# Performance work log

Measured on AMD Instinct MI355X. Metric: run time of the kernel, lower is better.

The kernel has to match this reference:

```python
import jax, jax.numpy as jnp
import numpy as np

B, N, D_MODEL = 2, 2048, 1024
H, HEAD_DIM, D1 = 16, 128, 2048
NK, RANK = 16, 32
GAMMA = 0.999


def setup_inputs() -> dict:
    key = jax.random.key(0)
    ks = jax.random.split(key, 12)
    std = 0.02
    return {
        "x": jax.random.normal(ks[0], (B, N, D_MODEL), jnp.float32),
        "Wu": jax.random.normal(ks[1], (D_MODEL, D1), jnp.float32) * std,
        "bu": jax.random.normal(ks[2], (D1,), jnp.float32) * std,
        "Wv": jax.random.normal(ks[3], (D_MODEL, D1), jnp.float32) * std,
        "bv": jax.random.normal(ks[4], (D1,), jnp.float32) * std,
        "Wo": jax.random.normal(ks[5], (D1, D_MODEL), jnp.float32) * std,
        "bo": jax.random.normal(ks[6], (D_MODEL,), jnp.float32) * std,
        # SKI low-rank Toeplitz kernel factors at nk inducing relative positions
        "a_pos": jax.random.normal(ks[7], (H, NK, RANK), jnp.float32) * 0.1,
        "b_pos": jax.random.normal(ks[8], (H, RANK, HEAD_DIM), jnp.float32) * 0.1,
        "a_neg": jax.random.normal(ks[9], (H, NK, RANK), jnp.float32) * 0.1,
        "b_neg": jax.random.normal(ks[10], (H, RANK, HEAD_DIM), jnp.float32) * 0.1,
        "t_zero": jax.random.normal(ks[11], (H, HEAD_DIM), jnp.float32) * 0.1,
    }


def _interp_decay_kernel(a, b, n):
    # low-rank kernel at nk inducing points: [h, nk, d]
    k_ind = jnp.einsum("hkr,hrd->hkd", a, b)
    lags = jnp.arange(1, n)                      # lags 1..n-1
    p = (lags - 1.0) / (n - 2.0) * (NK - 1)      # map lag onto inducing grid
    lo = jnp.floor(p).astype(jnp.int32)
    hi = jnp.minimum(lo + 1, NK - 1)
    w = (p - lo)[None, :, None]
    k = k_ind[:, lo, :] * (1.0 - w) + k_ind[:, hi, :] * w  # [h, n-1, d]
    decay = (GAMMA ** lags)[None, :, None]
    return k * decay


def reference(x, Wu, bu, Wv, bv, Wo, bo, a_pos, b_pos, a_neg, b_neg, t_zero):
    u = jax.nn.silu(x @ Wu + bu)                 # [b, n, d1]
    v = jax.nn.silu(x @ Wv + bv)                 # [b, n, d1]
    n = v.shape[1]
    vh = v.reshape(v.shape[0], n, H, HEAD_DIM)   # [b, n, h, d]

    kp = _interp_decay_kernel(a_pos, b_pos, n)   # [h, n-1, d]
    kn = _interp_decay_kernel(a_neg, b_neg, n)   # [h, n-1, d]
    m = 2 * n
    k_full = jnp.zeros((H, m, HEAD_DIM), vh.dtype)
    k_full = k_full.at[:, 0].set(t_zero)
    k_full = k_full.at[:, 1:n].set(kp)
    k_full = k_full.at[:, m - jnp.arange(1, n)].set(kn)  # non-causal (negative lags)

    # circular FFT convolution along the sequence axis
    vf = jnp.fft.rfft(vh, n=m, axis=1)                    # [b, mf, h, d]
    kf = jnp.transpose(jnp.fft.rfft(k_full, axis=1), (1, 0, 2))[None]  # [1, mf, h, d]
    y = jnp.fft.irfft(vf * kf, n=m, axis=1)[:, :n]        # [b, n, h, d]

    out = u * y.reshape(y.shape[0], n, D1)                # elementwise gate
    return out @ Wo + bo
```

## Files before the change

kernel.cpp:

```cpp
#include <hip/hip_runtime.h>
#include <hip/hip_bf16.h>
#include <stdint.h>
#include <stddef.h>

#define BB 2
#define NSEQ 2048
#define DM 1024
#define H 16
#define HD 128
#define D1 2048
#define NKI 16
#define RANKI 32
#define MROWS (BB * NSEQ)
#define VPROWS 6144
#define NTAP 28
#define NPAIR 13
#define NCHUNK 128
#define CLEN 16
#define GAMMA_F 0.999f
#define G_CL 0.9841201f
#define LN_G (-1.00050033e-3f)

__device__ constexpr int TAPS[NTAP] = {
  1, 2, 138, 139, 274, 275, 411, 412, 547, 548, 684,
  820, 821, 956, 957, 1093, 1094, 1229, 1230, 1366,
  1502, 1503, 1638, 1639, 1775, 1776, 1911, 1912};
__device__ constexpr int LEADL[NPAIR] = {1, 138, 274, 411, 547, 820, 956, 1093, 1229, 1502, 1638, 1775, 1911};
__device__ constexpr int LEADI[NPAIR] = {0, 2, 4, 6, 8, 11, 13, 15, 17, 20, 22, 24, 26};
#define SGL0_L 684
#define SGL0_I 10
#define SGL1_L 1366
#define SGL1_I 19

typedef short short8 __attribute__((ext_vector_type(8)));
typedef float floatx4 __attribute__((ext_vector_type(4)));

__device__ __forceinline__ float bf2f(unsigned short u) {
  union { unsigned int i; float f; } v; v.i = ((unsigned int)u) << 16; return v.f;
}
__device__ __forceinline__ unsigned short f2bf(float f) {
  union { float f; unsigned int i; } v; v.f = f;
  unsigned int r = (v.i + 0x7FFFu + ((v.i >> 16) & 1u)) >> 16;
  return (unsigned short)r;
}
__device__ __forceinline__ float bflo(unsigned int p) {
  union { unsigned int i; float f; } v; v.i = p << 16; return v.f;
}
__device__ __forceinline__ float bfhi(unsigned int p) {
  union { unsigned int i; float f; } v; v.i = p & 0xffff0000u; return v.f;
}
__device__ __forceinline__ void async16(const unsigned short* g, unsigned short* l) {
  __builtin_amdgcn_global_load_lds(
      (const __attribute__((address_space(1))) unsigned int*)g,
      (__attribute__((address_space(3))) unsigned int*)l, 16, 0, 0);
}

#define CVT4 (MROWS * DM / 4)
#define PAD16 (4 * NSEQ * D1 / 8)
__global__ __launch_bounds__(256) void prep_kernel(const float* __restrict__ x,
                                                   unsigned short* __restrict__ x_bf,
                                                   unsigned short* __restrict__ Vp) {
  int i = blockIdx.x * 256 + threadIdx.x;
  if (i < CVT4) {
    float4 f = ((const float4*)x)[i];
    ushort4 o;
    o.x = f2bf(f.x); o.y = f2bf(f.y); o.z = f2bf(f.z); o.w = f2bf(f.w);
    ((ushort4*)x_bf)[i] = o;
  } else {
    int j = i - CVT4;
    if (j < PAD16) {
      int r = j >> 19;
      int off = j & 524287;
      const size_t bases[4] = {0, (size_t)4096 * D1, (size_t)VPROWS * D1,
                               (size_t)VPROWS * D1 + (size_t)4096 * D1};
      uint4 z; z.x = z.y = z.z = z.w = 0u;
      ((uint4*)(Vp + bases[r]))[off] = z;
    }
  }
}

__device__ __forceinline__ float KinterpL(const float* kk, int l, int d) {
  if (l < 1) return 0.0f;
  float p = (float)(l - 1) * (15.0f / 2046.0f);
  int lo = (int)p; if (lo > 15) lo = 15;
  int hi = lo + 1; if (hi > 15) hi = 15;
  float w = p - (float)lo;
  float v = kk[lo * HD + d] * (1.0f - w) + kk[hi * HD + d] * w;
  return v * __powf(GAMMA_F, (float)l);
}

__global__ __launch_bounds__(256) void wprep_kernel(const float* __restrict__ Wu,
                                                    const float* __restrict__ Wv,
                                                    const float* __restrict__ Wo,
                                                    unsigned short* __restrict__ WT2,
                                                    unsigned short* __restrict__ WoT,
                                                    const float* __restrict__ ap,
                                                    const float* __restrict__ bp,
                                                    const float* __restrict__ an,
                                                    const float* __restrict__ bn,
                                                    float* __restrict__ dtp,
                                                    float* __restrict__ dtn) {
  int blk = blockIdx.x;
  int tid = threadIdx.x;
  if (blk < 6144) {
    __shared__ unsigned short t[32][33];
    const float* in; unsigned short* out;
    int rows, cols, bx, by;
    if (blk < 2048) {
      in = Wo; out = WoT; rows = D1; cols = DM;
      bx = (blk & 31) * 32; by = (blk >> 5) * 32;
    } else {
      int local = blk - 2048;
      int z = local >> 11, l2 = local & 2047;
      in = z ? Wv : Wu; out = WT2 + (size_t)z * D1 * DM;
      rows = DM; cols = D1;
      bx = (l2 & 63) * 32; by = (l2 >> 6) * 32;
    }
    int tx = tid & 31, ty = tid >> 5;
#pragma unroll
    for (int j = 0; j < 32; j += 8)
      t[ty + j][tx] = f2bf(in[(size_t)(by + ty + j) * cols + bx + tx]);
    __syncthreads();
#pragma unroll
    for (int j = 0; j < 32; j += 8)
      out[(size_t)(bx + ty + j) * rows + by + tx] = t[tx][ty + j];
  } else {
    __shared__ float kk[NKI * HD];
    int e0 = blk - 6144;
    int h = e0 & 15, dir = e0 >> 4;
    const float* a = (dir ? an : ap) + h * NKI * RANKI;
    const float* b = (dir ? bn : bp) + h * RANKI * HD;
    for (int e = tid; e < NKI * HD; e += 256) {
      int k = e >> 7, d = e & 127;
      float s = 0.0f;
#pragma unroll
      for (int r = 0; r < RANKI; ++r) s += a[k * RANKI + r] * b[r * HD + d];
      kk[e] = s;
    }
    __syncthreads();
    float* dt = (dir ? dtn : dtp) + (size_t)h * NTAP * HD;
    for (int e = tid; e < NTAP * HD; e += 256) {
      int j = e >> 7, d = e & 127;
      int l = TAPS[j];
      float K0 = KinterpL(kk, l, d);
      float K1 = KinterpL(kk, l - 1, d);
      float K2 = KinterpL(kk, l - 2, d);
      dt[e] = K0 - 2.0f * GAMMA_F * K1 + (GAMMA_F * GAMMA_F) * K2;
    }
  }
}

template <int MTILES>
__global__ __launch_bounds__(256) void gemm_uv(const unsigned short* __restrict__ A,
                                               const unsigned short* __restrict__ Bt,
                                               const float* __restrict__ bias,
                                               const float* __restrict__ bias2,
                                               void* __restrict__ C,
                                               void* __restrict__ C2,
                                               int M, int N, int K,
                                               int do_silu, int c_fp32, int uv_mode) {
  __shared__ unsigned short Al[2][MTILES * 1024];
  __shared__ unsigned short Bl[2][4096];
  int m0 = blockIdx.y * (MTILES * 32), n0 = blockIdx.x * 128;
  int tid = threadIdx.x;
  int lane = tid & 63, w = tid >> 6;
  int rw = (w >> 1) * (MTILES * 16), cw = (w & 1) * 64;
  int q = lane >> 4, l16 = lane & 15;
  floatx4 acc[MTILES][4];
#pragma unroll
  for (int mt = 0; mt < MTILES; ++mt)
#pragma unroll
    for (int nt = 0; nt < 4; ++nt) acc[mt][nt] = (floatx4){0.f, 0.f, 0.f, 0.f};
  int grow = tid >> 2;
  int gcol = (tid & 3) * 8;
  const unsigned short* A0 = A + (size_t)(m0 + grow) * K + gcol;
  const unsigned short* A1 = A0 + (size_t)64 * K;
  const unsigned short* B0 = Bt + (size_t)(n0 + grow) * K + gcol;
  const unsigned short* B1 = B0 + (size_t)64 * K;
  int woff = w * 512;
  int nIter = K >> 5;
  async16(A0, &Al[0][woff]);
  if (MTILES == 4) async16(A1, &Al[0][2048 + woff]);
  async16(B0, &Bl[0][woff]);
  async16(B1, &Bl[0][2048 + woff]);
  int p = 0;
  for (int i = 0; i < nIter; ++i) {
    __syncthreads();
    if (i + 1 < nIter) {
      int kn = (i + 1) << 5;
      async16(A0 + kn, &Al[p ^ 1][woff]);
      if (MTILES == 4) async16(A1 + kn, &Al[p ^ 1][2048 + woff]);
      async16(B0 + kn, &Bl[p ^ 1][woff]);
      async16(B1 + kn, &Bl[p ^ 1][2048 + woff]);
    }
    short8 af[MTILES], bfr[4];
#pragma unroll
    for (int i4 = 0; i4 < MTILES; ++i4)
      af[i4] = *(const short8*)(&Al[p][(rw + i4 * 16 + l16) * 32 + q * 8]);
#pragma unroll
    for (int i4 = 0; i4 < 4; ++i4)
      bfr[i4] = *(const short8*)(&Bl[p][(cw + i4 * 16 + l16) * 32 + q * 8]);
#pragma unroll
    for (int mt = 0; mt < MTILES; ++mt)
#pragma unroll
      for (int nt = 0; nt < 4; ++nt)
        acc[mt][nt] = __builtin_amdgcn_mfma_f32_16x16x32_bf16(af[mt], bfr[nt], acc[mt][nt], 0, 0, 0);
    p ^= 1;
  }
  int isv = uv_mode && (n0 >= 2048);
  int ldc = uv_mode ? 2048 : N;
  int ncb = isv ? (n0 - 2048) : n0;
  const float* buse = isv ? bias2 : bias;
#pragma unroll
  for (int mt = 0; mt < MTILES; ++mt) {
#pragma unroll
    for (int nt = 0; nt < 4; ++nt) {
      int n = ncb + cw + nt * 16 + l16;
      float bsv = buse[n];
#pragma unroll
      for (int r = 0; r < 4; ++r) {
        int m = m0 + rw + mt * 16 + q * 4 + r;
        float val = acc[mt][nt][r] + bsv;
        if (do_silu) val = val / (1.0f + __expf(-val));
        if (isv) {
          size_t mrow = (size_t)(2048 + m + ((m >> 11) << 12));
          ((unsigned short*)C2)[mrow * 2048 + n] = f2bf(val);
        } else if (c_fp32) {
          ((float*)C)[(size_t)m * ldc + n] = val;
        } else {
          ((unsigned short*)C)[(size_t)m * ldc + n] = f2bf(val);
        }
      }
    }
  }
}

template <int MTILES, int KCH>
__global__ __launch_bounds__(256) void gemm_out(const unsigned short* __restrict__ A,
                                                const unsigned short* __restrict__ Bt,
                                                const float* __restrict__ bias,
                                                float* __restrict__ C,
                                                int M, int N, int K) {
  constexpr int AREG = MTILES * 1024;
  constexpr int BREG = 4096;
  __shared__ unsigned short Al[2][AREG * KCH];
  __shared__ unsigned short Bl[2][BREG * KCH];
  int m0 = blockIdx.y * (MTILES * 32), n0 = blockIdx.x * 128;
  int tid = threadIdx.x;
  int lane = tid & 63, w = tid >> 6;
  int rw = (w >> 1) * (MTILES * 16), cw = (w & 1) * 64;
  int q = lane >> 4, l16 = lane & 15;
  floatx4 acc[MTILES][4];
#pragma unroll
  for (int mt = 0; mt < MTILES; ++mt)
#pragma unroll
    for (int nt = 0; nt < 4; ++nt) acc[mt][nt] = (floatx4){0.f, 0.f, 0.f, 0.f};
  int grow = tid >> 2;
  int gcol = (tid & 3) * 8;
  const unsigned short* A0 = A + (size_t)(m0 + grow) * K + gcol;
  const unsigned short* A1 = A0 + (size_t)64 * K;
  const unsigned short* B0 = Bt + (size_t)(n0 + grow) * K + gcol;
  const unsigned short* B1 = B0 + (size_t)64 * K;
  int woff = w * 512;
  int nIter = K / (32 * KCH);
#pragma unroll
  for (int kc = 0; kc < KCH; ++kc) {
    async16(A0 + kc * 32, &Al[0][kc * AREG + woff]);
    if (MTILES == 4) async16(A1 + kc * 32, &Al[0][kc * AREG + 2048 + woff]);
    async16(B0 + kc * 32, &Bl[0][kc * BREG + woff]);
    async16(B1 + kc * 32, &Bl[0][kc * BREG + 2048 + woff]);
  }
  int p = 0;
  for (int i = 0; i < nIter; ++i) {
    __syncthreads();
    if (i + 1 < nIter) {
      int kn = (i + 1) * 32 * KCH;
#pragma unroll
      for (int kc = 0; kc < KCH; ++kc) {
        async16(A0 + kn + kc * 32, &Al[p ^ 1][kc * AREG + woff]);
        if (MTILES == 4) async16(A1 + kn + kc * 32, &Al[p ^ 1][kc * AREG + 2048 + woff]);
        async16(B0 + kn + kc * 32, &Bl[p ^ 1][kc * BREG + woff]);
        async16(B1 + kn + kc * 32, &Bl[p ^ 1][kc * BREG + 2048 + woff]);
      }
    }
#pragma unroll
    for (int kc = 0; kc < KCH; ++kc) {
      short8 af[MTILES], bfr[4];
#pragma unroll
      for (int i4 = 0; i4 < MTILES; ++i4)
        af[i4] = *(const short8*)(&Al[p][kc * AREG + (rw + i4 * 16 + l16) * 32 + q * 8]);
#pragma unroll
      for (int i4 = 0; i4 < 4; ++i4)
        bfr[i4] = *(const short8*)(&Bl[p][kc * BREG + (cw + i4 * 16 + l16) * 32 + q * 8]);
#pragma unroll
      for (int mt = 0; mt < MTILES; ++mt)
#pragma unroll
        for (int nt = 0; nt < 4; ++nt)
          acc[mt][nt] = __builtin_amdgcn_mfma_f32_16x16x32_bf16(af[mt], bfr[nt], acc[mt][nt], 0, 0, 0);
    }
    p ^= 1;
  }
#pragma unroll
  for (int mt = 0; mt < MTILES; ++mt) {
#pragma unroll
    for (int nt = 0; nt < 4; ++nt) {
      int n = n0 + cw + nt * 16 + l16;
      float bsv = bias[n];
#pragma unroll
      for (int r = 0; r < 4; ++r) {
        int m = m0 + rw + mt * 16 + q * 4 + r;
        C[(size_t)m * N + n] = acc[mt][nt][r] + bsv;
      }
    }
  }
}

__global__ __launch_bounds__(256, 1) void scan_chunks(const unsigned short* __restrict__ Vp,
                                                      const float* __restrict__ dp,
                                                      const float* __restrict__ dn,
                                                      unsigned short* __restrict__ ypl,
                                                      unsigned short* __restrict__ ynl,
                                                      float* __restrict__ Sy_ex,
                                                      float* __restrict__ SG_ex) {
  int z = blockIdx.z;
  int dir = z >> 1, b = z & 1;
  int chunk = blockIdx.y;
  int c0 = blockIdx.x * 512 + threadIdx.x * 2;
  int h = c0 >> 7, d = c0 & 127;
  const float* dt = (dir ? dn : dp) + ((size_t)h * NTAP) * HD + d;
  float2 dreg[NTAP];
#pragma unroll
  for (int j = 0; j < NTAP; ++j) dreg[j] = *(const float2*)(dt + j * HD);
  const unsigned short* Vb = Vp + (size_t)b * VPROWS * D1 + c0;
  unsigned short* yl = (dir ? ynl : ypl) + (size_t)b * NSEQ * D1 + c0;
  float sy0 = 0.f, sy1 = 0.f, sg0 = 0.f, sg1 = 0.f;
  float carry0[NPAIR], carry1[NPAIR];
  if (!dir) {
    int t0 = chunk * CLEN;
    const unsigned short* Vrow = Vb + (size_t)(2048 + t0) * D1;
#pragma unroll
    for (int p = 0; p < NPAIR; ++p) {
      unsigned int pk = *(const unsigned int*)(Vrow - (ptrdiff_t)(LEADL[p] + 1) * D1);
      carry0[p] = bflo(pk); carry1[p] = bfhi(pk);
    }
    for (int i = 0; i < CLEN; ++i) {
      float F0 = 0.f, F1 = 0.f;
#pragma unroll
      for (int p = 0; p < NPAIR; ++p) {
        unsigned int pk = *(const unsigned int*)(Vrow - (ptrdiff_t)LEADL[p] * D1);
        float vl0 = bflo(pk), vl1 = bfhi(pk);
        F0 += dreg[LEADI[p]].x * vl0 + dreg[LEADI[p] + 1].x * carry0[p];
        F1 += dreg[LEADI[p]].y * vl1 + dreg[LEADI[p] + 1].y * carry1[p];
        carry0[p] = vl0; carry1[p] = vl1;
      }
      {
        unsigned int pk = *(const unsigned int*)(Vrow - (ptrdiff_t)SGL0_L * D1);
        F0 += dreg[SGL0_I].x * bflo(pk); F1 += dreg[SGL0_I].y * bfhi(pk);
      }
      {
        unsigned int pk = *(const unsigned int*)(Vrow - (ptrdiff_t)SGL1_L * D1);
        F0 += dreg[SGL1_I].x * bflo(pk); F1 += dreg[SGL1_I].y * bfhi(pk);
      }
      sg0 = GAMMA_F * sg0 + F0; sy0 = GAMMA_F * sy0 + sg0;
      sg1 = GAMMA_F * sg1 + F1; sy1 = GAMMA_F * sy1 + sg1;
      unsigned int pack = (unsigned int)f2bf(sy0) | ((unsigned int)f2bf(sy1) << 16);
      *(unsigned int*)(yl + (size_t)(t0 + i) * D1) = pack;
      Vrow += D1;
    }
  } else {
    int tstart = (NSEQ - 1) - chunk * CLEN;
    const unsigned short* Vrow = Vb + (size_t)(2048 + tstart) * D1;
#pragma unroll
    for (int p = 0; p < NPAIR; ++p) {
      unsigned int pk = *(const unsigned int*)(Vrow + (ptrdiff_t)(LEADL[p] + 1) * D1);
      carry0[p] = bflo(pk); carry1[p] = bfhi(pk);
    }
    for (int i = 0; i < CLEN; ++i) {
      float F0 = 0.f, F1 = 0.f;
#pragma unroll
      for (int p = 0; p < NPAIR; ++p) {
        unsigned int pk = *(const unsigned int*)(Vrow + (ptrdiff_t)LEADL[p] * D1);
        float vl0 = bflo(pk), vl1 = bfhi(pk);
        F0 += dreg[LEADI[p]].x * vl0 + dreg[LEADI[p] + 1].x * carry0[p];
        F1 += dreg[LEADI[p]].y * vl1 + dreg[LEADI[p] + 1].y * carry1[p];
        carry0[p] = vl0; carry1[p] = vl1;
      }
      {
        unsigned int pk = *(const unsigned int*)(Vrow + (ptrdiff_t)SGL0_L * D1);
        F0 += dreg[SGL0_I].x * bflo(pk); F1 += dreg[SGL0_I].y * bfhi(pk);
      }
      {
        unsigned int pk = *(const unsigned int*)(Vrow + (ptrdiff_t)SGL1_L * D1);
        F0 += dreg[SGL1_I].x * bflo(pk); F1 += dreg[SGL1_I].y * bfhi(pk);
      }
      sg0 = GAMMA_F * sg0 + F0; sy0 = GAMMA_F * sy0 + sg0;
      sg1 = GAMMA_F * sg1 + F1; sy1 = GAMMA_F * sy1 + sg1;
      unsigned int pack = (unsigned int)f2bf(sy0) | ((unsigned int)f2bf(sy1) << 16);
      *(unsigned int*)(yl + (size_t)(tstart - i) * D1) = pack;
      Vrow -= D1;
    }
  }
  size_t sidx = ((size_t)z * NCHUNK + chunk) * D1 + c0;
  Sy_ex[sidx] = sy0; Sy_ex[sidx + 1] = sy1;
  SG_ex[sidx] = sg0; SG_ex[sidx + 1] = sg1;
}

__global__ __launch_bounds__(256) void state_scan(const float* __restrict__ Sy_ex,
                                                  const float* __restrict__ SG_ex,
                                                  float* __restrict__ Sy_in,
                                                  float* __restrict__ SG_in) {
  int idx = blockIdx.x * 256 + threadIdx.x;
  if (idx >= 4 * D1) return;
  int z = idx >> 11, c = idx & (D1 - 1);
  float ey = 0.f, eg = 0.f;
  for (int k = 0; k < NCHUNK; ++k) {
    size_t s = ((size_t)z * NCHUNK + k) * D1 + c;
    Sy_in[s] = ey; SG_in[s] = eg;
    float lex = Sy_ex[s], lgx = SG_ex[s];
    ey = lex + G_CL * (ey + (float)CLEN * eg);
    eg = lgx + G_CL * eg;
  }
}

__global__ __launch_bounds__(256) void combine_kernel(const unsigned short* __restrict__ ypl,
                                                      const unsigned short* __restrict__ ynl,
                                                      const unsigned short* __restrict__ Vp,
                                                      const float* __restrict__ Sy_in,
                                                      const float* __restrict__ SG_in,
                                                      const float* __restrict__ tz,
                                                      const unsigned short* __restrict__ U,
                                                      unsigned short* __restrict__ G) {
  int e = blockIdx.x * 256 + threadIdx.x;
  int cq = e & (D1 / 4 - 1);
  int c0 = cq * 4;
  int r = e >> 9;
  int t = r & (NSEQ - 1);
  int b = r >> 11;
  int kp = t >> 4;  float dpD = (float)((t & 15) + 1);
  int tau = (NSEQ - 1) - t;
  int kn = tau >> 4; float dnD = (float)((tau & 15) + 1);
  float gp = __expf(dpD * LN_G);
  float gn = __expf(dnD * LN_G);
  size_t ix = (size_t)r * D1 + c0;
  size_t sp = ((size_t)(b) * NCHUNK + kp) * D1 + c0;
  size_t sn = ((size_t)(2 + b) * NCHUNK + kn) * D1 + c0;
  uint2 pyl = *(const uint2*)(ypl + ix);
  uint2 pyn = *(const uint2*)(ynl + ix);
  uint2 pv  = *(const uint2*)(Vp + ((size_t)b * VPROWS + 2048 + t) * D1 + c0);
  uint2 pu  = *(const uint2*)(U + ix);
  float4 syp = *(const float4*)(Sy_in + sp);
  float4 sgp = *(const float4*)(SG_in + sp);
  float4 syn = *(const float4*)(Sy_in + sn);
  float4 sgn = *(const float4*)(SG_in + sn);
  float4 tzv = *(const float4*)(tz + c0);
  float yv[4], uv[4], vv[4];
  yv[0] = bflo(pyl.x) + gp * (syp.x + dpD * sgp.x) + bflo(pyn.x) + gn * (syn.x + dnD * sgn.x);
  yv[1] = bfhi(pyl.x) + gp * (syp.y + dpD * sgp.y) + bfhi(pyn.x) + gn * (syn.y + dnD * sgn.y);
  yv[2] = bflo(pyl.y) + gp * (syp.z + dpD * sgp.z) + bflo(pyn.y) + gn * (syn.z + dnD * sgn.z);
  yv[3] = bfhi(pyl.y) + gp * (syp.w + dpD * sgp.w) + bfhi(pyn.y) + gn * (syn.w + dnD * sgn.w);
  vv[0] = bflo(pv.x); vv[1] = bfhi(pv.x); vv[2] = bflo(pv.y); vv[3] = bfhi(pv.y);
  uv[0] = bflo(pu.x); uv[1] = bfhi(pu.x); uv[2] = bflo(pu.y); uv[3] = bfhi(pu.y);
  float tza[4] = {tzv.x, tzv.y, tzv.z, tzv.w};
  uint2 og;
  unsigned short g0 = f2bf(uv[0] * (yv[0] + tza[0] * vv[0]));
  unsigned short g1 = f2bf(uv[1] * (yv[1] + tza[1] * vv[1]));
  unsigned short g2 = f2bf(uv[2] * (yv[2] + tza[2] * vv[2]));
  unsigned short g3 = f2bf(uv[3] * (yv[3] + tza[3] * vv[3]));
  og.x = (unsigned int)g0 | ((unsigned int)g1 << 16);
  og.y = (unsigned int)g2 | ((unsigned int)g3 << 16);
  *(uint2*)(G + ix) = og;
}

extern "C" void kernel_launch(void* const* d_in, const int* in_sizes, int n_in,
                              void* d_out, int out_size, void* d_ws, size_t ws_size,
                              hipStream_t stream) {
  const float* x      = (const float*)d_in[0];
  const float* Wu     = (const float*)d_in[1];
  const float* bu     = (const float*)d_in[2];
  const float* Wv     = (const float*)d_in[3];
  const float* bv     = (const float*)d_in[4];
  const float* Wo     = (const float*)d_in[5];
  const float* bo     = (const float*)d_in[6];
  const float* a_pos  = (const float*)d_in[7];
  const float* b_pos  = (const float*)d_in[8];
  const float* a_neg  = (const float*)d_in[9];
  const float* b_neg  = (const float*)d_in[10];
  const float* t_zero = (const float*)d_in[11];
  float* out = (float*)d_out;

  char* ws = (char*)d_ws;
  unsigned short* x_bf  = (unsigned short*)ws; ws += (size_t)MROWS * DM * 2;
  unsigned short* u_ws  = (unsigned short*)ws; ws += (size_t)MROWS * D1 * 2;
  unsigned short* Vp    = (unsigned short*)ws; ws += (size_t)BB * VPROWS * D1 * 2;
  unsigned short* ypl   = (unsigned short*)ws; ws += (size_t)MROWS * D1 * 2;
  unsigned short* ynl   = (unsigned short*)ws; ws += (size_t)MROWS * D1 * 2;
  unsigned short* WoT   = (unsigned short*)ws; ws += (size_t)DM * D1 * 2;
  float* dtp   = (float*)ws; ws += (size_t)H * NTAP * HD * 4;
  float* dtn   = (float*)ws; ws += (size_t)H * NTAP * HD * 4;
  float* Sy_in = (float*)ws; ws += (size_t)4 * NCHUNK * D1 * 4;
  float* SG_in = (float*)ws; ws += (size_t)4 * NCHUNK * D1 * 4;
  float* Sy_ex = (float*)x_bf;
  float* SG_ex = (float*)x_bf + (size_t)4 * NCHUNK * D1;
  unsigned short* WT2 = ypl;

  dim3 tb256(256);
  prep_kernel<<<dim3((CVT4 + PAD16 + 255) / 256), tb256, 0, stream>>>(x, x_bf, Vp);
  wprep_kernel<<<dim3(6176), tb256, 0, stream>>>(
      Wu, Wv, Wo, WT2, WoT, a_pos, b_pos, a_neg, b_neg, dtp, dtn);
  gemm_uv<4><<<dim3(2 * D1 / 128, MROWS / 128), tb256, 0, stream>>>(
      x_bf, WT2, bu, bv, u_ws, Vp, MROWS, 2 * D1, DM, 1, 0, 1);
  scan_chunks<<<dim3(D1 / 512, NCHUNK, 4), tb256, 0, stream>>>(Vp, dtp, dtn, ypl, ynl, Sy_ex, SG_ex);
  state_scan<<<dim3((4 * D1 + 255) / 256), tb256, 0, stream>>>(Sy_ex, SG_ex, Sy_in, SG_in);
  combine_kernel<<<dim3((size_t)MROWS * D1 / 1024), tb256, 0, stream>>>(ypl, ynl, Vp, Sy_in, SG_in, t_zero, u_ws, u_ws);
  gemm_out<2, 2><<<dim3(DM / 128, MROWS / 64), tb256, 0, stream>>>(
      u_ws, WoT, bo, out, MROWS, DM, D1);
}
```

Before: 297.9 us.

## Replace uv GEMM with 256x256-tile 512-thread kernel using swizzled LDS

Replaces the 128x128-tile, 256-thread u/v projection GEMM with a specialized kernel. Each 512-thread block computes a 256x256 tile with a BK=64 double-buffered LDS pipeline that keeps two stages in flight. It also XOR-swizzles the LDS layout to avoid bank conflicts, remaps block indices for L2 locality, and raises wave priority around the MFMA bursts. The intent is higher arithmetic intensity per byte loaded and better MFMA utilization. The cost is heavy register pressure (128 accumulator floats per thread) and 128KB of LDS per block, which limits occupancy.

```diff
diff --git a/kernel.cpp b/kernel.cpp
--- a/kernel.cpp
+++ b/kernel.cpp
@@ -150,85 +150,123 @@
   }
 }
 
-template <int MTILES>
-__global__ __launch_bounds__(256) void gemm_uv(const unsigned short* __restrict__ A,
-                                               const unsigned short* __restrict__ Bt,
-                                               const float* __restrict__ bias,
-                                               const float* __restrict__ bias2,
-                                               void* __restrict__ C,
-                                               void* __restrict__ C2,
-                                               int M, int N, int K,
-                                               int do_silu, int c_fp32, int uv_mode) {
-  __shared__ unsigned short Al[2][MTILES * 1024];
-  __shared__ unsigned short Bl[2][4096];
-  int m0 = blockIdx.y * (MTILES * 32), n0 = blockIdx.x * 128;
+__global__ __launch_bounds__(512) void gemm_uv8(const unsigned short* __restrict__ A,
+                                                const unsigned short* __restrict__ Bt,
+                                                const float* __restrict__ bu,
+                                                const float* __restrict__ bv,
+                                                unsigned short* __restrict__ U,
+                                                unsigned short* __restrict__ Vp) {
+  __shared__ unsigned short lds[65536];
+  constexpr int K = DM;
+  constexpr int NT = K / 64;
+  int lin = blockIdx.y * 16 + blockIdx.x;
+  int swz = (lin & 7) * 32 + (lin >> 3);
+  int n0 = (swz & 15) * 256;
+  int m0 = (swz >> 4) * 256;
   int tid = threadIdx.x;
   int lane = tid & 63, w = tid >> 6;
-  int rw = (w >> 1) * (MTILES * 16), cw = (w & 1) * 64;
+  int wm = w >> 2, wn = w & 3;
   int q = lane >> 4, l16 = lane & 15;
-  floatx4 acc[MTILES][4];
-#pragma unroll
-  for (int mt = 0; mt < MTILES; ++mt)
-#pragma unroll
-    for (int nt = 0; nt < 4; ++nt) acc[mt][nt] = (floatx4){0.f, 0.f, 0.f, 0.f};
-  int grow = tid >> 2;
-  int gcol = (tid & 3) * 8;
-  const unsigned short* A0 = A + (size_t)(m0 + grow) * K + gcol;
-  const unsigned short* A1 = A0 + (size_t)64 * K;
-  const unsigned short* B0 = Bt + (size_t)(n0 + grow) * K + gcol;
-  const unsigned short* B1 = B0 + (size_t)64 * K;
-  int woff = w * 512;
-  int nIter = K >> 5;
-  async16(A0, &Al[0][woff]);
-  if (MTILES == 4) async16(A1, &Al[0][2048 + woff]);
-  async16(B0, &Bl[0][woff]);
-  async16(B1, &Bl[0][2048 + woff]);
-  int p = 0;
-  for (int i = 0; i < nIter; ++i) {
-    __syncthreads();
-    if (i + 1 < nIter) {
-      int kn = (i + 1) << 5;
-      async16(A0 + kn, &Al[p ^ 1][woff]);
-      if (MTILES == 4) async16(A1 + kn, &Al[p ^ 1][2048 + woff]);
-      async16(B0 + kn, &Bl[p ^ 1][woff]);
-      async16(B1 + kn, &Bl[p ^ 1][2048 + woff]);
-    }
-    short8 af[MTILES], bfr[4];
-#pragma unroll
-    for (int i4 = 0; i4 < MTILES; ++i4)
-      af[i4] = *(const short8*)(&Al[p][(rw + i4 * 16 + l16) * 32 + q * 8]);
-#pragma unroll
-    for (int i4 = 0; i4 < 4; ++i4)
-      bfr[i4] = *(const short8*)(&Bl[p][(cw + i4 * 16 + l16) * 32 + q * 8]);
-#pragma unroll
-    for (int mt = 0; mt < MTILES; ++mt)
-#pragma unroll
-      for (int nt = 0; nt < 4; ++nt)
-        acc[mt][nt] = __builtin_amdgcn_mfma_f32_16x16x32_bf16(af[mt], bfr[nt], acc[mt][nt], 0, 0, 0);
-    p ^= 1;
-  }
-  int isv = uv_mode && (n0 >= 2048);
-  int ldc = uv_mode ? 2048 : N;
-  int ncb = isv ? (n0 - 2048) : n0;
-  const float* buse = isv ? bias2 : bias;
-#pragma unroll
-  for (int mt = 0; mt < MTILES; ++mt) {
-#pragma unroll
-    for (int nt = 0; nt < 4; ++nt) {
-      int n = ncb + cw + nt * 16 + l16;
-      float bsv = buse[n];
+  int srow = lane >> 3;
+  int soff = ((lane & 7) ^ srow) << 3;
+  const unsigned short* Ab = A + (size_t)(m0 + w * 8 + srow) * K + soff;
+  const unsigned short* Bb = Bt + (size_t)(n0 + w * 8 + srow) * K + soff;
+  unsigned aoff0 = w * 512;
+  unsigned boff0 = 32768u + w * 512;
+  int swk0 = (q ^ (l16 & 7)) << 3;
+  int swk1 = ((4 | q) ^ (l16 & 7)) << 3;
+  int pAr = wm * 8192;
+  int pBr = 32768 + (wn >> 1) * 8192;
+  int rB0 = (wn & 1) * 64;
+
+  floatx4 acc[8][4];
+#pragma unroll
+  for (int f = 0; f < 8; ++f)
+#pragma unroll
+    for (int g = 0; g < 4; ++g) acc[f][g] = (floatx4){0.f, 0.f, 0.f, 0.f};
+
+  auto stage = [&](int p, int t) {
+    const unsigned short* a = Ab + t * 64;
+    const unsigned short* b = Bb + t * 64;
+    unsigned ao = aoff0 + p * 16384;
+    unsigned bo = boff0 + p * 16384;
+    async16(a,               &lds[ao]);
+    async16(a + (size_t)64 * K,  &lds[ao + 4096]);
+    async16(a + (size_t)128 * K, &lds[ao + 8192]);
+    async16(a + (size_t)192 * K, &lds[ao + 12288]);
+    async16(b,               &lds[bo]);
+    async16(b + (size_t)64 * K,  &lds[bo + 4096]);
+    async16(b + (size_t)128 * K, &lds[bo + 8192]);
+    async16(b + (size_t)192 * K, &lds[bo + 12288]);
+  };
+
+  stage(0, 0);
+  stage(1, 1);
+  asm volatile("s_waitcnt vmcnt(8)" ::: "memory");
+  __builtin_amdgcn_s_barrier();
+
+  for (int t = 0; t < NT; ++t) {
+    int p = t & 1;
+    const unsigned short* As = &lds[pAr + p * 16384];
+    const unsigned short* Bs = &lds[pBr + p * 16384];
+#pragma unroll
+    for (int mh = 0; mh < 2; ++mh) {
+      short8 af[4][2], bfr[4][2];
+#pragma unroll
+      for (int f = 0; f < 4; ++f) {
+        int rh = ((mh * 4 + f) * 16 + l16) * 64;
+        af[f][0] = *(const short8*)(As + rh + swk0);
+        af[f][1] = *(const short8*)(As + rh + swk1);
+      }
+#pragma unroll
+      for (int g = 0; g < 4; ++g) {
+        int rh = (rB0 + g * 16 + l16) * 64;
+        bfr[g][0] = *(const short8*)(Bs + rh + swk0);
+        bfr[g][1] = *(const short8*)(Bs + rh + swk1);
+      }
+      __builtin_amdgcn_s_setprio(1);
+#pragma unroll
+      for (int f = 0; f < 4; ++f)
+#pragma unroll
+        for (int g = 0; g < 4; ++g) {
+          acc[mh * 4 + f][g] = __builtin_amdgcn_mfma_f32_16x16x32_bf16(
+              af[f][0], bfr[g][0], acc[mh * 4 + f][g], 0, 0, 0);
+          acc[mh * 4 + f][g] = __builtin_amdgcn_mfma_f32_16x16x32_bf16(
+              af[f][1], bfr[g][1], acc[mh * 4 + f][g], 0, 0, 0);
+        }
+      __builtin_amdgcn_s_setprio(0);
+    }
+    if (t == NT - 1) break;
+    asm volatile("" ::: "memory");
+    __builtin_amdgcn_s_barrier();
+    if (t + 2 < NT) {
+      stage(p, t + 2);
+      asm volatile("s_waitcnt vmcnt(8)" ::: "memory");
+    } else {
+      asm volatile("s_waitcnt vmcnt(0)" ::: "memory");
+    }
+    __builtin_amdgcn_s_barrier();
+  }
+
+  int isv = (n0 >= 2048);
+  const float* bias = isv ? bv : bu;
+#pragma unroll
+  for (int f = 0; f < 8; ++f) {
+#pragma unroll
+    for (int g = 0; g < 4; ++g) {
+      int n = n0 + wn * 64 + g * 16 + l16;
+      int nc = isv ? (n - 2048) : n;
+      float bsv = bias[nc];
 #pragma unroll
       for (int r = 0; r < 4; ++r) {
-        int m = m0 + rw + mt * 16 + q * 4 + r;
-        float val = acc[mt][nt][r] + bsv;
-        if (do_silu) val = val / (1.0f + __expf(-val));
+        int m = m0 + wm * 128 + f * 16 + q * 4 + r;
+        float val = acc[f][g][r] + bsv;
+        val = val / (1.0f + __expf(-val));
         if (isv) {
           size_t mrow = (size_t)(2048 + m + ((m >> 11) << 12));
-          ((unsigned short*)C2)[mrow * 2048 + n] = f2bf(val);
-        } else if (c_fp32) {
-          ((float*)C)[(size_t)m * ldc + n] = val;
+          Vp[mrow * 2048 + nc] = f2bf(val);
         } else {
-          ((unsigned short*)C)[(size_t)m * ldc + n] = f2bf(val);
+          U[(size_t)m * 2048 + nc] = f2bf(val);
         }
       }
     }
@@ -507,8 +545,7 @@
   prep_kernel<<<dim3((CVT4 + PAD16 + 255) / 256), tb256, 0, stream>>>(x, x_bf, Vp);
   wprep_kernel<<<dim3(6176), tb256, 0, stream>>>(
       Wu, Wv, Wo, WT2, WoT, a_pos, b_pos, a_neg, b_neg, dtp, dtn);
-  gemm_uv<4><<<dim3(2 * D1 / 128, MROWS / 128), tb256, 0, stream>>>(
-      x_bf, WT2, bu, bv, u_ws, Vp, MROWS, 2 * D1, DM, 1, 0, 1);
+  gemm_uv8<<<dim3(16, 16), dim3(512), 0, stream>>>(x_bf, WT2, bu, bv, u_ws, Vp);
   scan_chunks<<<dim3(D1 / 512, NCHUNK, 4), tb256, 0, stream>>>(Vp, dtp, dtn, ypl, ynl, Sy_ex, SG_ex);
   state_scan<<<dim3((4 * D1 + 255) / 256), tb256, 0, stream>>>(Sy_ex, SG_ex, Sy_in, SG_in);
   combine_kernel<<<dim3((size_t)MROWS * D1 / 1024), tb256, 0, stream>>>(ypl, ynl, Vp, Sy_in, SG_in, t_zero, u_ws, u_ws);
```

Measured after the change: 276.2 us. -7.3%, faster.
